# Optimization experiments

Hardware: AMD Instinct MI355X
Metric: run time of the kernel (lower is better)

## Reference

```python
import jax, jax.numpy as jnp
import numpy as np

NUM_USERS = 100000
NUM_ITEMS = 50000
N_NODES = NUM_USERS + NUM_ITEMS
EMBED_DIM = 64
NUM_LAYERS = 3
NUM_EDGES = 1250000
EDGE_ATTR_DIM = 7
MLP_HID = 32
AUDIO_SCALE = 1.0
META_SCALE = 0.5


def _l2norm(x, eps=1e-12):
    # F.normalize(p=2, dim=-1): x / max(||x||, eps)
    n = jnp.sqrt(jnp.sum(x * x, axis=-1, keepdims=True))
    return x / jnp.maximum(n, eps)


def setup_inputs() -> dict:
    key = jax.random.key(0)
    ks = jax.random.split(key, 12)
    return {
        'user_emb_w': jax.random.normal(ks[0], (NUM_USERS, EMBED_DIM), jnp.float32),
        'artist_emb_w': jax.random.normal(ks[1], (20000, EMBED_DIM), jnp.float32),
        'album_emb_w': jax.random.normal(ks[2], (40000, EMBED_DIM), jnp.float32),
        'item_audio': jax.random.normal(ks[3], (NUM_ITEMS, EMBED_DIM), jnp.float32),
        'edge_attr': jax.random.normal(ks[4], (NUM_EDGES, EDGE_ATTR_DIM), jnp.float32),
        'edge_weight_init': jax.random.uniform(ks[5], (NUM_EDGES,), jnp.float32),
        'w1': jax.random.normal(ks[6], (EDGE_ATTR_DIM + 1, MLP_HID), jnp.float32),
        'b1': jnp.zeros((MLP_HID,), jnp.float32),
        'w2': jax.random.normal(ks[7], (MLP_HID, 1), jnp.float32),
        'b2': jnp.zeros((1,), jnp.float32),
        'edge_index': jax.random.randint(ks[8], (2, NUM_EDGES), 0, N_NODES, jnp.int64 if jax.config.read('jax_enable_x64') else jnp.int32),
        'artist_ids': jax.random.randint(ks[9], (NUM_ITEMS,), 0, 20000, jnp.int32),
        'album_ids': jax.random.randint(ks[10], (NUM_ITEMS,), 0, 40000, jnp.int32),
    }


def reference(user_emb_w, artist_emb_w, album_emb_w, item_audio, edge_attr,
              edge_weight_init, w1, b1, w2, b2, edge_index, artist_ids, album_ids):
    # Edge weight MLP: Linear -> ReLU -> Linear -> Sigmoid, squeezed
    ef = jnp.concatenate([edge_attr, edge_weight_init[:, None]], axis=1)  # [E, 8]
    h = jax.nn.relu(ef @ w1 + b1)
    w = jax.nn.sigmoid(h @ w2 + b2)[:, 0]  # [E]

    # Node features
    user_embed = _l2norm(user_emb_w)                                   # [U, D]
    meta = (artist_emb_w[artist_ids] + album_emb_w[album_ids]) * META_SCALE
    item_embed = _l2norm(item_audio * AUDIO_SCALE + meta)              # [I, D]
    x = jnp.concatenate([user_embed, item_embed], axis=0)              # [N, D]

    # gcn_norm (LGConv default, no self-loops): deg from target (col) scatter of w
    row, col = edge_index[0], edge_index[1]
    deg = jax.ops.segment_sum(w, col, num_segments=N_NODES)
    dinv = jnp.where(deg > 0, jax.lax.rsqrt(jnp.maximum(deg, 1e-30)), 0.0)
    norm = dinv[row] * w * dinv[col]                                   # [E]

    acc = x
    for _ in range(NUM_LAYERS):
        msg = norm[:, None] * x[row]                                   # [E, D]
        x = jax.ops.segment_sum(msg, col, num_segments=N_NODES)       # [N, D]
        acc = acc + x
    x = _l2norm(acc / (NUM_LAYERS + 1))

    user_emb = x[:NUM_USERS]
    item_emb = x[NUM_USERS:]
    align_loss = jnp.float32(0.0)
    return user_emb, item_emb, align_loss
```

## Files before the change

### kernel.cpp

```cpp
#include <hip/hip_runtime.h>
#include <hip/hip_bf16.h>
#include <math.h>

#define NUM_USERS  100000
#define NUM_ITEMS  50000
#define N_NODES    150000
#define EMBED_DIM  64
#define NUM_EDGES  1250000
#define MLP_HID    32
#define SCAN_B     1024
#define SCAN_NB    ((N_NODES + SCAN_B - 1) / SCAN_B)
#define NPW        4
#define PAD(x)     (((x) + 15) & ~15)

__global__ void hist_mlp(const float* __restrict__ edge_attr,
                         const float* __restrict__ ew,
                         const float* __restrict__ w1,
                         const float* __restrict__ b1,
                         const float* __restrict__ w2,
                         const float* __restrict__ b2,
                         const int*   __restrict__ edge_index,
                         int*   __restrict__ cnt,
                         float* __restrict__ deg,
                         int*   __restrict__ rank,
                         int2*  __restrict__ epair) {
    __shared__ float w1s[8 * MLP_HID];
    __shared__ float b1s[MLP_HID];
    __shared__ float w2s[MLP_HID];
    int tid = threadIdx.x;
    if (tid < 8 * MLP_HID) w1s[tid] = w1[tid];
    if (tid < MLP_HID) { b1s[tid] = b1[tid]; w2s[tid] = w2[tid]; }
    __syncthreads();

    int e = blockIdx.x * blockDim.x + tid;
    if (e >= NUM_EDGES) return;

    int c = edge_index[NUM_EDGES + e];
    rank[e] = atomicAdd(&cnt[c], 1);

    float ef[8];
#pragma unroll
    for (int k = 0; k < 7; ++k) ef[k] = edge_attr[e * 7 + k];
    ef[7] = ew[e];

    float s = b2[0];
#pragma unroll
    for (int j = 0; j < MLP_HID; ++j) {
        float h = b1s[j];
#pragma unroll
        for (int k = 0; k < 8; ++k) h = fmaf(ef[k], w1s[k * MLP_HID + j], h);
        h = fmaxf(h, 0.0f);
        s = fmaf(h, w2s[j], s);
    }
    float w = 1.0f / (1.0f + expf(-s));

    atomicAdd(&deg[c], w);

    int2 pr;
    pr.x = edge_index[e];
    pr.y = __float_as_int(w);
    epair[e] = pr;
}

__global__ void scan_partial(const int* __restrict__ cnt,
                             int* __restrict__ part) {
    __shared__ int s[SCAN_B];
    int tid = threadIdx.x;
    int i = blockIdx.x * SCAN_B + tid;
    s[tid] = (i < N_NODES) ? PAD(cnt[i]) : 0;
    __syncthreads();
#pragma unroll
    for (int off = SCAN_B / 2; off > 0; off >>= 1) {
        if (tid < off) s[tid] += s[tid + off];
        __syncthreads();
    }
    if (tid == 0) part[blockIdx.x] = s[0];
}

__global__ void scan_offsets(const int* __restrict__ part,
                             int* __restrict__ base_off) {
    __shared__ int s[256];
    int tid = threadIdx.x;
    int v = (tid < SCAN_NB) ? part[tid] : 0;
    s[tid] = v;
    __syncthreads();
#pragma unroll
    for (int off = 1; off < 256; off <<= 1) {
        int t = (tid >= off) ? s[tid - off] : 0;
        __syncthreads();
        s[tid] += t;
        __syncthreads();
    }
    if (tid < SCAN_NB) base_off[tid] = s[tid] - v;
}

__global__ void scan_apply(const int* __restrict__ cnt,
                           const int* __restrict__ base_off,
                           int* __restrict__ row_ptr) {
    __shared__ int s[SCAN_B];
    int tid = threadIdx.x;
    int i = blockIdx.x * SCAN_B + tid;
    int v = (i < N_NODES) ? PAD(cnt[i]) : 0;
    s[tid] = v;
    __syncthreads();
    for (int off = 1; off < SCAN_B; off <<= 1) {
        int t = (tid >= off) ? s[tid - off] : 0;
        __syncthreads();
        s[tid] += t;
        __syncthreads();
    }
    if (i < N_NODES) row_ptr[i] = s[tid] - v + base_off[blockIdx.x];
    if (i == N_NODES - 1) row_ptr[N_NODES] = s[tid] + base_off[blockIdx.x];
}

__global__ void make_dinv(const float* __restrict__ deg,
                          float* __restrict__ dinv,
                          const int* __restrict__ row_ptr,
                          int2* __restrict__ csr_pair) {
    int t = blockIdx.x * blockDim.x + threadIdx.x;
    if (t < N_NODES) {
        float d = deg[t];
        dinv[t] = (d > 0.0f) ? rsqrtf(fmaxf(d, 1e-30f)) : 0.0f;
    }
    if (t < 64) {
        int end = row_ptr[N_NODES];
        int2 z; z.x = 0; z.y = 0;
        csr_pair[end + t] = z;
    }
}

__global__ void scatter_perm(const int* __restrict__ edge_index,
                             const int* __restrict__ rank,
                             const int* __restrict__ row_ptr,
                             int* __restrict__ perm) {
    int e = blockIdx.x * blockDim.x + threadIdx.x;
    if (e >= NUM_EDGES) return;
    int c = edge_index[NUM_EDGES + e];
    perm[row_ptr[c] + rank[e]] = e;
}

__global__ void pair_build(const int* __restrict__ row_ptr,
                           const int* __restrict__ cnt,
                           const int* __restrict__ perm,
                           const int2* __restrict__ epair,
                           const float* __restrict__ dinv,
                           int2* __restrict__ csr_pair) {
    int t = blockIdx.x * blockDim.x + threadIdx.x;
    int node = t >> 4;
    int lane = t & 15;
    if (node >= N_NODES) return;
    int s = row_ptr[node];
    int e = row_ptr[node + 1];
    int re = s + cnt[node];
    float dc = dinv[node];
    for (int j = s + lane; j < e; j += 16) {
        int2 pr;
        if (j < re) {
            int eid = perm[j];
            pr = epair[eid];
            pr.y = __float_as_int(__int_as_float(pr.y) * dc * dinv[pr.x]);
        } else {
            pr.x = 0; pr.y = 0;
        }
        csr_pair[j] = pr;
    }
}

__global__ void init_x(const float* __restrict__ user_w,
                       const float* __restrict__ artist_w,
                       const float* __restrict__ album_w,
                       const float* __restrict__ audio,
                       const int*   __restrict__ artist_ids,
                       const int*   __restrict__ album_ids,
                       __hip_bfloat16* __restrict__ x) {
    int t = blockIdx.x * blockDim.x + threadIdx.x;
    int row = t >> 6;
    int lane = t & 63;
    if (row >= N_NODES) return;

    float v;
    if (row < NUM_USERS) {
        v = user_w[row * EMBED_DIM + lane];
    } else {
        int r = row - NUM_USERS;
        int ar = artist_ids[r];
        int al = album_ids[r];
        v = audio[r * EMBED_DIM + lane]
          + 0.5f * (artist_w[ar * EMBED_DIM + lane] + album_w[al * EMBED_DIM + lane]);
    }
    float ss = v * v;
#pragma unroll
    for (int off = 32; off > 0; off >>= 1) ss += __shfl_xor(ss, off);
    float scale = 1.0f / fmaxf(sqrtf(ss), 1e-12f);
    x[row * EMBED_DIM + lane] = __float2bfloat16(v * scale);
}

#define BF_LO(u) __uint_as_float((u) << 16)
#define BF_HI(u) __uint_as_float((u) & 0xffff0000u)

#define REDUCE_ACC()                                                         \
    a0 += __shfl_xor(a0, 16); a1 += __shfl_xor(a1, 16);                      \
    a2 += __shfl_xor(a2, 16); a3 += __shfl_xor(a3, 16);                      \
    a0 += __shfl_xor(a0, 32); a1 += __shfl_xor(a1, 32);                      \
    a2 += __shfl_xor(a2, 32); a3 += __shfl_xor(a3, 32)

#define NEXT_BOUND() ((k == 1) ? rs2 : (k == 2) ? rs3 : rs4)

__global__ void propagate_mid(const int* __restrict__ row_ptr,
                              const int2* __restrict__ csr_pair,
                              const unsigned short* __restrict__ xin,
                              unsigned short* __restrict__ xout) {
    int wave = (blockIdx.x * blockDim.x + threadIdx.x) >> 6;
    int lane = threadIdx.x & 63;
    int node0 = wave * NPW;
    if (node0 >= N_NODES) return;

    int eg = lane >> 4;
    int dq = (lane & 15) << 2;

    int rpv = row_ptr[node0 + (lane <= NPW ? lane : NPW)];
    int rs0 = __shfl(rpv, 0);
    int rs1 = __shfl(rpv, 1);
    int rs2 = __shfl(rpv, 2);
    int rs3 = __shfl(rpv, 3);
    int rs4 = __shfl(rpv, 4);

    float a0 = 0, a1 = 0, a2 = 0, a3 = 0;
    int k = 0;
    int bnext = rs1;

#define STORE_MID()                                                          \
    do {                                                                     \
        if (eg == 0) {                                                       \
            size_t o = ((size_t)(node0 + k) << 6) + dq;                      \
            unsigned int b0 = (unsigned int)__bfloat16_as_ushort(__float2bfloat16(a0)); \
            unsigned int b1 = (unsigned int)__bfloat16_as_ushort(__float2bfloat16(a1)); \
            unsigned int b2 = (unsigned int)__bfloat16_as_ushort(__float2bfloat16(a2)); \
            unsigned int b3 = (unsigned int)__bfloat16_as_ushort(__float2bfloat16(a3)); \
            uint2 u;                                                         \
            u.x = b0 | (b1 << 16);                                           \
            u.y = b2 | (b3 << 16);                                           \
            *(uint2*)(xout + o) = u;                                         \
        }                                                                    \
    } while (0)

    while (k < NPW && rs0 == bnext) {
        STORE_MID();
        ++k;
        bnext = NEXT_BOUND();
    }

    int j = rs0 + (eg << 2);
    int2 pa0 = csr_pair[j],      pa1 = csr_pair[j + 1];
    int2 pa2 = csr_pair[j + 2],  pa3 = csr_pair[j + 3];
    uint2 ua0 = *(const uint2*)(xin + ((size_t)pa0.x << 6) + dq);
    uint2 ua1 = *(const uint2*)(xin + ((size_t)pa1.x << 6) + dq);
    uint2 ua2 = *(const uint2*)(xin + ((size_t)pa2.x << 6) + dq);
    uint2 ua3 = *(const uint2*)(xin + ((size_t)pa3.x << 6) + dq);
    int2 pb0 = csr_pair[j + 16], pb1 = csr_pair[j + 17];
    int2 pb2 = csr_pair[j + 18], pb3 = csr_pair[j + 19];

    for (int base = rs0; base < rs4; base += 16) {
        bool live = (base + 16) < rs4;
        int sb0 = live ? pb0.x : 0;
        int sb1 = live ? pb1.x : 0;
        int sb2 = live ? pb2.x : 0;
        int sb3 = live ? pb3.x : 0;
        uint2 ub0 = *(const uint2*)(xin + ((size_t)sb0 << 6) + dq);
        uint2 ub1 = *(const uint2*)(xin + ((size_t)sb1 << 6) + dq);
        uint2 ub2 = *(const uint2*)(xin + ((size_t)sb2 << 6) + dq);
        uint2 ub3 = *(const uint2*)(xin + ((size_t)sb3 << 6) + dq);
        int2 pc0 = csr_pair[j + 32], pc1 = csr_pair[j + 33];
        int2 pc2 = csr_pair[j + 34], pc3 = csr_pair[j + 35];

        float w0 = __int_as_float(pa0.y);
        float w1 = __int_as_float(pa1.y);
        float w2 = __int_as_float(pa2.y);
        float w3 = __int_as_float(pa3.y);
        a0 = fmaf(w0, BF_LO(ua0.x), a0); a1 = fmaf(w0, BF_HI(ua0.x), a1);
        a2 = fmaf(w0, BF_LO(ua0.y), a2); a3 = fmaf(w0, BF_HI(ua0.y), a3);
        a0 = fmaf(w1, BF_LO(ua1.x), a0); a1 = fmaf(w1, BF_HI(ua1.x), a1);
        a2 = fmaf(w1, BF_LO(ua1.y), a2); a3 = fmaf(w1, BF_HI(ua1.y), a3);
        a0 = fmaf(w2, BF_LO(ua2.x), a0); a1 = fmaf(w2, BF_HI(ua2.x), a1);
        a2 = fmaf(w2, BF_LO(ua2.y), a2); a3 = fmaf(w2, BF_HI(ua2.y), a3);
        a0 = fmaf(w3, BF_LO(ua3.x), a0); a1 = fmaf(w3, BF_HI(ua3.x), a1);
        a2 = fmaf(w3, BF_LO(ua3.y), a2); a3 = fmaf(w3, BF_HI(ua3.y), a3);

        pa0 = pb0; pa1 = pb1; pa2 = pb2; pa3 = pb3;
        pb0 = pc0; pb1 = pc1; pb2 = pc2; pb3 = pc3;
        ua0 = ub0; ua1 = ub1; ua2 = ub2; ua3 = ub3;
        j += 16;

        int pos = base + 16;
        while (k < NPW && pos == bnext) {
            REDUCE_ACC();
            STORE_MID();
            a0 = 0; a1 = 0; a2 = 0; a3 = 0;
            ++k;
            bnext = NEXT_BOUND();
        }
    }
#undef STORE_MID
}

__global__ void propagate_final(const int* __restrict__ row_ptr,
                                const int2* __restrict__ csr_pair,
                                const unsigned short* __restrict__ x0,
                                const unsigned short* __restrict__ x1,
                                const unsigned short* __restrict__ x2,
                                float* __restrict__ outp) {
    int wave = (blockIdx.x * blockDim.x + threadIdx.x) >> 6;
    int lane = threadIdx.x & 63;
    int node0 = wave * NPW;
    if (node0 >= N_NODES) return;

    int eg = lane >> 4;
    int dq = (lane & 15) << 2;

    int rpv = row_ptr[node0 + (lane <= NPW ? lane : NPW)];
    int rs0 = __shfl(rpv, 0);
    int rs1 = __shfl(rpv, 1);
    int rs2 = __shfl(rpv, 2);
    int rs3 = __shfl(rpv, 3);
    int rs4 = __shfl(rpv, 4);

    float a0 = 0, a1 = 0, a2 = 0, a3 = 0;
    int k = 0;
    int bnext = rs1;

#define STORE_FIN()                                                          \
    do {                                                                     \
        if (eg == 0) {                                                       \
            size_t o = ((size_t)(node0 + k) << 6) + dq;                      \
            uint2 u0 = *(const uint2*)(x0 + o);                              \
            uint2 u1 = *(const uint2*)(x1 + o);                              \
            uint2 u2 = *(const uint2*)(x2 + o);                              \
            float v0 = (BF_LO(u0.x) + BF_LO(u1.x) + BF_LO(u2.x) + a0) * 0.25f; \
            float v1 = (BF_HI(u0.x) + BF_HI(u1.x) + BF_HI(u2.x) + a1) * 0.25f; \
            float v2 = (BF_LO(u0.y) + BF_LO(u1.y) + BF_LO(u2.y) + a2) * 0.25f; \
            float v3 = (BF_HI(u0.y) + BF_HI(u1.y) + BF_HI(u2.y) + a3) * 0.25f; \
            float ss = v0 * v0 + v1 * v1 + v2 * v2 + v3 * v3;                \
            ss += __shfl_xor(ss, 1);                                         \
            ss += __shfl_xor(ss, 2);                                         \
            ss += __shfl_xor(ss, 4);                                         \
            ss += __shfl_xor(ss, 8);                                         \
            float scale = 1.0f / fmaxf(sqrtf(ss), 1e-12f);                   \
            float4 r = { v0 * scale, v1 * scale, v2 * scale, v3 * scale };   \
            *(float4*)(outp + o) = r;                                        \
        }                                                                    \
    } while (0)

    while (k < NPW && rs0 == bnext) {
        STORE_FIN();
        ++k;
        bnext = NEXT_BOUND();
    }

    int j = rs0 + (eg << 2);
    int2 pa0 = csr_pair[j],      pa1 = csr_pair[j + 1];
    int2 pa2 = csr_pair[j + 2],  pa3 = csr_pair[j + 3];
    uint2 ua0 = *(const uint2*)(x2 + ((size_t)pa0.x << 6) + dq);
    uint2 ua1 = *(const uint2*)(x2 + ((size_t)pa1.x << 6) + dq);
    uint2 ua2 = *(const uint2*)(x2 + ((size_t)pa2.x << 6) + dq);
    uint2 ua3 = *(const uint2*)(x2 + ((size_t)pa3.x << 6) + dq);
    int2 pb0 = csr_pair[j + 16], pb1 = csr_pair[j + 17];
    int2 pb2 = csr_pair[j + 18], pb3 = csr_pair[j + 19];

    for (int base = rs0; base < rs4; base += 16) {
        bool live = (base + 16) < rs4;
        int sb0 = live ? pb0.x : 0;
        int sb1 = live ? pb1.x : 0;
        int sb2 = live ? pb2.x : 0;
        int sb3 = live ? pb3.x : 0;
        uint2 ub0 = *(const uint2*)(x2 + ((size_t)sb0 << 6) + dq);
        uint2 ub1 = *(const uint2*)(x2 + ((size_t)sb1 << 6) + dq);
        uint2 ub2 = *(const uint2*)(x2 + ((size_t)sb2 << 6) + dq);
        uint2 ub3 = *(const uint2*)(x2 + ((size_t)sb3 << 6) + dq);
        int2 pc0 = csr_pair[j + 32], pc1 = csr_pair[j + 33];
        int2 pc2 = csr_pair[j + 34], pc3 = csr_pair[j + 35];

        float w0 = __int_as_float(pa0.y);
        float w1 = __int_as_float(pa1.y);
        float w2 = __int_as_float(pa2.y);
        float w3 = __int_as_float(pa3.y);
        a0 = fmaf(w0, BF_LO(ua0.x), a0); a1 = fmaf(w0, BF_HI(ua0.x), a1);
        a2 = fmaf(w0, BF_LO(ua0.y), a2); a3 = fmaf(w0, BF_HI(ua0.y), a3);
        a0 = fmaf(w1, BF_LO(ua1.x), a0); a1 = fmaf(w1, BF_HI(ua1.x), a1);
        a2 = fmaf(w1, BF_LO(ua1.y), a2); a3 = fmaf(w1, BF_HI(ua1.y), a3);
        a0 = fmaf(w2, BF_LO(ua2.x), a0); a1 = fmaf(w2, BF_HI(ua2.x), a1);
        a2 = fmaf(w2, BF_LO(ua2.y), a2); a3 = fmaf(w2, BF_HI(ua2.y), a3);
        a0 = fmaf(w3, BF_LO(ua3.x), a0); a1 = fmaf(w3, BF_HI(ua3.x), a1);
        a2 = fmaf(w3, BF_LO(ua3.y), a2); a3 = fmaf(w3, BF_HI(ua3.y), a3);

        pa0 = pb0; pa1 = pb1; pa2 = pb2; pa3 = pb3;
        pb0 = pc0; pb1 = pc1; pb2 = pc2; pb3 = pc3;
        ua0 = ub0; ua1 = ub1; ua2 = ub2; ua3 = ub3;
        j += 16;

        int pos = base + 16;
        while (k < NPW && pos == bnext) {
            REDUCE_ACC();
            STORE_FIN();
            a0 = 0; a1 = 0; a2 = 0; a3 = 0;
            ++k;
            bnext = NEXT_BOUND();
        }
    }
#undef STORE_FIN
    if (blockIdx.x == 0 && threadIdx.x == 0)
        outp[(size_t)N_NODES * EMBED_DIM] = 0.0f;
}

#undef BF_LO
#undef BF_HI

extern "C" void kernel_launch(void* const* d_in, const int* in_sizes, int n_in,
                              void* d_out, int out_size, void* d_ws, size_t ws_size,
                              hipStream_t stream) {
    const float* user_w     = (const float*)d_in[0];
    const float* artist_w   = (const float*)d_in[1];
    const float* album_w    = (const float*)d_in[2];
    const float* audio      = (const float*)d_in[3];
    const float* edge_attr  = (const float*)d_in[4];
    const float* ew         = (const float*)d_in[5];
    const float* w1         = (const float*)d_in[6];
    const float* b1         = (const float*)d_in[7];
    const float* w2         = (const float*)d_in[8];
    const float* b2         = (const float*)d_in[9];
    const int*   edge_index = (const int*)d_in[10];
    const int*   artist_ids = (const int*)d_in[11];
    const int*   album_ids  = (const int*)d_in[12];
    float* out = (float*)d_out;

    float* ws = (float*)d_ws;
    unsigned short* x0 = (unsigned short*)ws;
    unsigned short* x1 = (unsigned short*)(ws + 4800000);
    unsigned short* x2 = (unsigned short*)(ws + 9600000);
    float* dinv    = ws + 14400000;
    int*  row_ptr  = (int*)(ws + 14560000);
    int2* csr_pair = (int2*)(ws + 14720000);
    int*   cnt     = (int*)ws;
    float* deg     = ws + 150000;
    int*   rank    = (int*)(ws + 300000);
    int*   part    = (int*)(ws + 1600000);
    int*   baseoff = (int*)(ws + 1601000);
    int2*  epair   = (int2*)(ws + 1700000);
    int*   perm    = (int*)(ws + 4800000);

    const int B = 256;
    const int egrid   = (NUM_EDGES + B - 1) / B;
    const int ngrid   = (N_NODES * EMBED_DIM) / B;
    const int ngrid16 = (N_NODES * 16) / B;
    const int dgrid   = (N_NODES + B - 1) / B;
    const int pgrid   = (N_NODES / NPW * 64) / B;

    hipMemsetAsync(cnt, 0, 2 * N_NODES * sizeof(int), stream);

    hist_mlp<<<egrid, B, 0, stream>>>(
        edge_attr, ew, w1, b1, w2, b2, edge_index, cnt, deg, rank, epair);

    scan_partial<<<SCAN_NB, SCAN_B, 0, stream>>>(cnt, part);
    scan_offsets<<<1, 256, 0, stream>>>(part, baseoff);
    scan_apply<<<SCAN_NB, SCAN_B, 0, stream>>>(cnt, baseoff, row_ptr);

    make_dinv<<<dgrid, B, 0, stream>>>(deg, dinv, row_ptr, csr_pair);

    scatter_perm<<<egrid, B, 0, stream>>>(edge_index, rank, row_ptr, perm);

    pair_build<<<ngrid16, B, 0, stream>>>(
        row_ptr, cnt, perm, epair, dinv, csr_pair);

    init_x<<<ngrid, B, 0, stream>>>(
        user_w, artist_w, album_w, audio, artist_ids, album_ids,
        (__hip_bfloat16*)x0);

    propagate_mid<<<pgrid, B, 0, stream>>>(row_ptr, csr_pair, x0, x1);
    propagate_mid<<<pgrid, B, 0, stream>>>(row_ptr, csr_pair, x1, x2);
    propagate_final<<<pgrid, B, 0, stream>>>(row_ptr, csr_pair, x0, x1, x2, out);
}
```

Before: 467.6 us.

## Compute degree from CSR segments instead of float atomics; thread-coarsen edge kernels

Removes the per-edge float atomicAdd into deg. Each node's degree is now summed inside pair_build with a 16-lane shuffle reduction over its CSR segment, and normalization moves into a new csr_scale_pad pass. hist_mlp handles two edges per thread and scatter_perm handles four. The catch is an extra read-modify-write pass over the CSR pair array.

```diff
diff --git a/kernel.cpp b/kernel.cpp
--- a/kernel.cpp
+++ b/kernel.cpp
@@ -21,7 +21,6 @@
                          const float* __restrict__ b2,
                          const int*   __restrict__ edge_index,
                          int*   __restrict__ cnt,
-                         float* __restrict__ deg,
                          int*   __restrict__ rank,
                          int2*  __restrict__ epair) {
     __shared__ float w1s[8 * MLP_HID];
@@ -32,34 +31,49 @@
     if (tid < MLP_HID) { b1s[tid] = b1[tid]; w2s[tid] = w2[tid]; }
     __syncthreads();
 
-    int e = blockIdx.x * blockDim.x + tid;
-    if (e >= NUM_EDGES) return;
-
-    int c = edge_index[NUM_EDGES + e];
-    rank[e] = atomicAdd(&cnt[c], 1);
-
-    float ef[8];
-#pragma unroll
-    for (int k = 0; k < 7; ++k) ef[k] = edge_attr[e * 7 + k];
-    ef[7] = ew[e];
-
-    float s = b2[0];
+    int t = blockIdx.x * blockDim.x + tid;
+    int e0 = 2 * t;
+    int e1 = 2 * t + 1;
+    if (e0 >= NUM_EDGES) return;
+
+    int c0 = edge_index[NUM_EDGES + e0];
+    int c1 = edge_index[NUM_EDGES + e1];
+    int r0 = atomicAdd(&cnt[c0], 1);
+    int r1 = atomicAdd(&cnt[c1], 1);
+
+    float ef0[8], ef1[8];
+#pragma unroll
+    for (int k = 0; k < 7; ++k) ef0[k] = edge_attr[e0 * 7 + k];
+#pragma unroll
+    for (int k = 0; k < 7; ++k) ef1[k] = edge_attr[e1 * 7 + k];
+    ef0[7] = ew[e0];
+    ef1[7] = ew[e1];
+
+    float s0 = b2[0], s1 = b2[0];
 #pragma unroll
     for (int j = 0; j < MLP_HID; ++j) {
-        float h = b1s[j];
-#pragma unroll
-        for (int k = 0; k < 8; ++k) h = fmaf(ef[k], w1s[k * MLP_HID + j], h);
-        h = fmaxf(h, 0.0f);
-        s = fmaf(h, w2s[j], s);
-    }
-    float w = 1.0f / (1.0f + expf(-s));
-
-    atomicAdd(&deg[c], w);
-
-    int2 pr;
-    pr.x = edge_index[e];
-    pr.y = __float_as_int(w);
-    epair[e] = pr;
+        float h0 = b1s[j], h1 = b1s[j];
+#pragma unroll
+        for (int k = 0; k < 8; ++k) {
+            float wv = w1s[k * MLP_HID + j];
+            h0 = fmaf(ef0[k], wv, h0);
+            h1 = fmaf(ef1[k], wv, h1);
+        }
+        h0 = fmaxf(h0, 0.0f);
+        h1 = fmaxf(h1, 0.0f);
+        float w2v = w2s[j];
+        s0 = fmaf(h0, w2v, s0);
+        s1 = fmaf(h1, w2v, s1);
+    }
+    float wa = 1.0f / (1.0f + expf(-s0));
+    float wb = 1.0f / (1.0f + expf(-s1));
+
+    rank[e0] = r0;
+    rank[e1] = r1;
+    int2 pr0; pr0.x = edge_index[e0]; pr0.y = __float_as_int(wa);
+    int2 pr1; pr1.x = edge_index[e1]; pr1.y = __float_as_int(wb);
+    epair[e0] = pr0;
+    epair[e1] = pr1;
 }
 
 __global__ void scan_partial(const int* __restrict__ cnt,
@@ -113,38 +127,26 @@
     if (i == N_NODES - 1) row_ptr[N_NODES] = s[tid] + base_off[blockIdx.x];
 }
 
-__global__ void make_dinv(const float* __restrict__ deg,
-                          float* __restrict__ dinv,
-                          const int* __restrict__ row_ptr,
-                          int2* __restrict__ csr_pair) {
-    int t = blockIdx.x * blockDim.x + threadIdx.x;
-    if (t < N_NODES) {
-        float d = deg[t];
-        dinv[t] = (d > 0.0f) ? rsqrtf(fmaxf(d, 1e-30f)) : 0.0f;
-    }
-    if (t < 64) {
-        int end = row_ptr[N_NODES];
-        int2 z; z.x = 0; z.y = 0;
-        csr_pair[end + t] = z;
-    }
-}
-
 __global__ void scatter_perm(const int* __restrict__ edge_index,
                              const int* __restrict__ rank,
                              const int* __restrict__ row_ptr,
                              int* __restrict__ perm) {
-    int e = blockIdx.x * blockDim.x + threadIdx.x;
+    int t = blockIdx.x * blockDim.x + threadIdx.x;
+    int e = 4 * t;
     if (e >= NUM_EDGES) return;
-    int c = edge_index[NUM_EDGES + e];
-    perm[row_ptr[c] + rank[e]] = e;
+#pragma unroll
+    for (int q = 0; q < 4; ++q) {
+        int c = edge_index[NUM_EDGES + e + q];
+        perm[row_ptr[c] + rank[e + q]] = e + q;
+    }
 }
 
 __global__ void pair_build(const int* __restrict__ row_ptr,
                            const int* __restrict__ cnt,
                            const int* __restrict__ perm,
                            const int2* __restrict__ epair,
-                           const float* __restrict__ dinv,
-                           int2* __restrict__ csr_pair) {
+                           int2* __restrict__ csr_pair,
+                           float* __restrict__ dinv) {
     int t = blockIdx.x * blockDim.x + threadIdx.x;
     int node = t >> 4;
     int lane = t & 15;
@@ -152,17 +154,43 @@
     int s = row_ptr[node];
     int e = row_ptr[node + 1];
     int re = s + cnt[node];
-    float dc = dinv[node];
+    float sum = 0.0f;
     for (int j = s + lane; j < e; j += 16) {
         int2 pr;
         if (j < re) {
             int eid = perm[j];
             pr = epair[eid];
-            pr.y = __float_as_int(__int_as_float(pr.y) * dc * dinv[pr.x]);
+            sum += __int_as_float(pr.y);
         } else {
             pr.x = 0; pr.y = 0;
         }
         csr_pair[j] = pr;
+    }
+    sum += __shfl_xor(sum, 8);
+    sum += __shfl_xor(sum, 4);
+    sum += __shfl_xor(sum, 2);
+    sum += __shfl_xor(sum, 1);
+    if (lane == 0)
+        dinv[node] = (sum > 0.0f) ? rsqrtf(fmaxf(sum, 1e-30f)) : 0.0f;
+    if (node == N_NODES - 1) {
+        int2 z; z.x = 0; z.y = 0;
+        for (int q = lane; q < 64; q += 16) csr_pair[e + q] = z;
+    }
+}
+
+__global__ void csr_scale_pad(const int* __restrict__ row_ptr,
+                              const float* __restrict__ dinv,
+                              int2* __restrict__ csr_pair) {
+    int t = blockIdx.x * blockDim.x + threadIdx.x;
+    int node = t >> 4;
+    int lane = t & 15;
+    if (node >= N_NODES) return;
+    int s = row_ptr[node], e = row_ptr[node + 1];
+    float dc = dinv[node];
+    for (int j = s + lane; j < e; j += 16) {
+        int2 p = csr_pair[j];
+        p.y = __float_as_int(__int_as_float(p.y) * dc * dinv[p.x]);
+        csr_pair[j] = p;
     }
 }
 
@@ -440,35 +468,34 @@
     int*  row_ptr  = (int*)(ws + 14560000);
     int2* csr_pair = (int2*)(ws + 14720000);
     int*   cnt     = (int*)ws;
-    float* deg     = ws + 150000;
-    int*   rank    = (int*)(ws + 300000);
+    int*   rank    = (int*)(ws + 150000);
     int*   part    = (int*)(ws + 1600000);
     int*   baseoff = (int*)(ws + 1601000);
     int2*  epair   = (int2*)(ws + 1700000);
     int*   perm    = (int*)(ws + 4800000);
 
     const int B = 256;
-    const int egrid   = (NUM_EDGES + B - 1) / B;
+    const int egrid2  = (NUM_EDGES / 2 + B - 1) / B;
+    const int egrid4  = (NUM_EDGES / 4 + B - 1) / B;
     const int ngrid   = (N_NODES * EMBED_DIM) / B;
     const int ngrid16 = (N_NODES * 16) / B;
-    const int dgrid   = (N_NODES + B - 1) / B;
     const int pgrid   = (N_NODES / NPW * 64) / B;
 
-    hipMemsetAsync(cnt, 0, 2 * N_NODES * sizeof(int), stream);
-
-    hist_mlp<<<egrid, B, 0, stream>>>(
-        edge_attr, ew, w1, b1, w2, b2, edge_index, cnt, deg, rank, epair);
+    hipMemsetAsync(cnt, 0, N_NODES * sizeof(int), stream);
+
+    hist_mlp<<<egrid2, B, 0, stream>>>(
+        edge_attr, ew, w1, b1, w2, b2, edge_index, cnt, rank, epair);
 
     scan_partial<<<SCAN_NB, SCAN_B, 0, stream>>>(cnt, part);
     scan_offsets<<<1, 256, 0, stream>>>(part, baseoff);
     scan_apply<<<SCAN_NB, SCAN_B, 0, stream>>>(cnt, baseoff, row_ptr);
 
-    make_dinv<<<dgrid, B, 0, stream>>>(deg, dinv, row_ptr, csr_pair);
-
-    scatter_perm<<<egrid, B, 0, stream>>>(edge_index, rank, row_ptr, perm);
+    scatter_perm<<<egrid4, B, 0, stream>>>(edge_index, rank, row_ptr, perm);
 
     pair_build<<<ngrid16, B, 0, stream>>>(
-        row_ptr, cnt, perm, epair, dinv, csr_pair);
+        row_ptr, cnt, perm, epair, csr_pair, dinv);
+
+    csr_scale_pad<<<ngrid16, B, 0, stream>>>(row_ptr, dinv, csr_pair);
 
     init_x<<<ngrid, B, 0, stream>>>(
         user_w, artist_w, album_w, audio, artist_ids, album_ids,
```

Result: faster. 421.9 us (-9.8%).
